# Kernel tuning notes

Hardware: AMD Instinct MI355X
Metric: run time of the kernel (lower is better)

Reference implementation:

```python
import jax, jax.numpy as jnp
import numpy as np

B, I, O, G = 262144, 3, 64, 128


def setup_inputs() -> dict:
    key = jax.random.key(0)
    kx, kc = jax.random.split(key)
    x = jax.random.uniform(kx, (1, B, I), dtype=jnp.float32)  # coords in [0,1)
    coeffs = jax.random.normal(kc, (2, O, I, G), dtype=jnp.float32) / (
        np.float32(np.sqrt(I) * np.sqrt(G))
    )
    bias = jnp.zeros((1, O), dtype=jnp.float32)
    return {"x": x, "coeffs": coeffs, "bias": bias}


def reference(x, coeffs, bias):
    # x: (1, B, I); coeffs: (2, O, I, G); bias: (1, O)
    b, i = x.shape[1], x.shape[2]
    two, o, _, g = coeffs.shape
    k = jnp.arange(1, g + 1, dtype=x.dtype)          # (G,)
    kx = x.reshape(b, i, 1) * k                      # (B, I, G)
    cosf = jnp.cos(kx).reshape(b, i * g)             # (B, I*G)
    sinf = jnp.sin(kx).reshape(b, i * g)             # (B, I*G)
    w = coeffs.reshape(2, o, i * g)                  # (2, O, I*G)
    # sum over (input_dim, gridsize) fused as one GEMM per trig branch
    out = cosf @ w[0].T + sinf @ w[1].T + bias       # (B, O)
    return out
```

## Files before the change

### kernel.cpp

```cpp
#include <hip/hip_runtime.h>
#include <hip/hip_bf16.h>

typedef __attribute__((ext_vector_type(8))) short short8;
typedef __attribute__((ext_vector_type(4))) float f32x4;
typedef __attribute__((ext_vector_type(2))) float f32x2;
typedef __attribute__((ext_vector_type(4))) unsigned int u32x4;

#define NROWS   262144
#define ODIM    64
#define NBLOCKS 256
#define TPB     1024
#define INV2PI  0.15915494309189535f

__device__ __forceinline__ float cos2pi(float f){ float r; asm("v_cos_f32 %0, %1" : "=v"(r) : "v"(f)); return r; }
__device__ __forceinline__ float sin2pi(float f){ float r; asm("v_sin_f32 %0, %1" : "=v"(r) : "v"(f)); return r; }
__device__ __forceinline__ unsigned pkbf(float lo, float hi){
    unsigned r; asm("v_cvt_pk_bf16_f32 %0, %1, %2" : "=v"(r) : "v"(lo), "v"(hi)); return r;
}
__device__ __forceinline__ short8 as_s8(u32x4 v){ union{u32x4 u; short8 s;} x; x.u = v; return x.s; }
__device__ __forceinline__ short bf16_of(float f){
    union { __hip_bfloat16 h; short s; } u; u.h = __float2bfloat16(f); return u.s;
}

extern "C" __global__ void __launch_bounds__(TPB, 4)
fourier_mfma(const float* __restrict__ x,
             const float* __restrict__ coeffs,
             const float* __restrict__ bias,
             float* __restrict__ out)
{
    __shared__ short8 Wlds[24 * 4 * 64];

    const int tid = threadIdx.x;

    for (int fl = tid; fl < 24*4*64; fl += TPB) {
        const int ks = fl >> 8;
        const int nt = (fl >> 6) & 3;
        const int ln = fl & 63;
        const int o  = nt*16 + (ln & 15);
        const int kg = ln >> 4;
        union { short8 v; short s[8]; } fr;
        #pragma unroll
        for (int h = 0; h < 2; ++h) {
            const int kb  = ks*32 + h*16;
            const int br  = (kb >= 384) ? 1 : 0;
            const int rem = kb - br*384;
            const int ii  = rem >> 7;
            const int g0  = (rem & 127) + kg*4;
            const float* wp = coeffs + (((br*ODIM + o)*3 + ii) << 7) + g0;
            #pragma unroll
            for (int j = 0; j < 4; ++j) fr.s[h*4 + j] = bf16_of(wp[j]);
        }
        Wlds[fl] = fr.v;
    }

    const int lane = tid & 63;
    const int wid  = tid >> 6;
    const int mrow = lane & 15;
    const int kgrp = lane >> 4;
    const float h0f = (float)(4*kgrp + 1);

    const int unit = blockIdx.x * 16 + wid;
    const int base = unit * 64;

    f32x2 xr[2][3];
    #pragma unroll
    for (int rg = 0; rg < 2; ++rg) {
        const int rowA = base + (rg*2 + 0)*16 + mrow;
        const int rowB = base + (rg*2 + 1)*16 + mrow;
        #pragma unroll
        for (int i = 0; i < 3; ++i)
            xr[rg][i] = (f32x2){ x[rowA*3 + i] * INV2PI, x[rowB*3 + i] * INV2PI };
    }
    float bcol[4];
    #pragma unroll
    for (int nt = 0; nt < 4; ++nt) bcol[nt] = bias[nt*16 + mrow];

    __syncthreads();

#define ANCHOR(RG, I) do {                                          \
    const f32x2 a = xr[RG][I];                                      \
    cv  = (f32x2){ cos2pi(a.x), cos2pi(a.y) };                      \
    sv  = (f32x2){ sin2pi(a.x), sin2pi(a.y) };                      \
    f32x2 t = (f32x2){ 16.f*a.x, 16.f*a.y };                        \
    t.x -= floorf(t.x); t.y -= floorf(t.y);                         \
    c16 = (f32x2){ cos2pi(t.x), cos2pi(t.y) };                      \
    s16 = (f32x2){ sin2pi(t.x), sin2pi(t.y) };                      \
    f32x2 u = (f32x2){ h0f*a.x, h0f*a.y };                          \
    u.x -= floorf(u.x); u.y -= floorf(u.y);                         \
    stc = (f32x2){ cos2pi(u.x), cos2pi(u.y) };                      \
    sts = (f32x2){ sin2pi(u.x), sin2pi(u.y) };                      \
} while (0)

#define HALF(D0, D1, FCA, FCB, FSA, FSB) do {                       \
    const f32x2 c0 = stc,        s0 = sts;                          \
    const f32x2 c1 = c0*cv - s0*sv, s1 = s0*cv + c0*sv;             \
    FCA.D0 = pkbf(c0.x, c1.x);  FCB.D0 = pkbf(c0.y, c1.y);          \
    FSA.D0 = pkbf(s0.x, s1.x);  FSB.D0 = pkbf(s0.y, s1.y);          \
    const f32x2 c2 = c1*cv - s1*sv, s2 = s1*cv + c1*sv;             \
    const f32x2 c3 = c2*cv - s2*sv, s3 = s2*cv + c2*sv;             \
    FCA.D1 = pkbf(c2.x, c3.x);  FCB.D1 = pkbf(c2.y, c3.y);          \
    FSA.D1 = pkbf(s2.x, s3.x);  FSB.D1 = pkbf(s2.y, s3.y);          \
    const f32x2 nc = stc*c16 - sts*s16, ns = sts*c16 + stc*s16;     \
    stc = nc; sts = ns;                                             \
} while (0)

#define FEAT(RG, KKP, FCA, FCB, FSA, FSB) do {                      \
    if (((KKP) & 3) == 0) ANCHOR(RG, (KKP) >> 2);                   \
    HALF(x, y, FCA, FCB, FSA, FSB);                                 \
    HALF(z, w, FCA, FCB, FSA, FSB);                                 \
} while (0)

    #pragma unroll
    for (int rg = 0; rg < 2; ++rg) {
        f32x4 acc[2][4];
        #pragma unroll
        for (int rr = 0; rr < 2; ++rr)
            #pragma unroll
            for (int nt = 0; nt < 4; ++nt)
                acc[rr][nt] = (f32x4){0.f, 0.f, 0.f, 0.f};

        f32x2 cv, sv, c16, s16, stc, sts;
        u32x4 F[2][4];

        FEAT(rg, 0, F[0][0], F[0][1], F[0][2], F[0][3]);

        #pragma unroll
        for (int kk = 0; kk < 12; ++kk) {
            const int cb = kk & 1;
            short8 bc[4], bs[4];
            #pragma unroll
            for (int nt = 0; nt < 4; ++nt) {
                bc[nt] = Wlds[(kk*4 + nt)*64 + lane];
                bs[nt] = Wlds[((kk + 12)*4 + nt)*64 + lane];
            }

            if (kk < 11)
                FEAT(rg, kk+1, F[cb^1][0], F[cb^1][1], F[cb^1][2], F[cb^1][3]);

            const short8 fAc = as_s8(F[cb][0]);
            const short8 fBc = as_s8(F[cb][1]);
            const short8 fAs = as_s8(F[cb][2]);
            const short8 fBs = as_s8(F[cb][3]);

            __builtin_amdgcn_s_setprio(1);
            #pragma unroll
            for (int nt = 0; nt < 4; ++nt) {
                acc[0][nt] = __builtin_amdgcn_mfma_f32_16x16x32_bf16(fAc, bc[nt], acc[0][nt], 0, 0, 0);
                acc[1][nt] = __builtin_amdgcn_mfma_f32_16x16x32_bf16(fBc, bc[nt], acc[1][nt], 0, 0, 0);
                acc[0][nt] = __builtin_amdgcn_mfma_f32_16x16x32_bf16(fAs, bs[nt], acc[0][nt], 0, 0, 0);
                acc[1][nt] = __builtin_amdgcn_mfma_f32_16x16x32_bf16(fBs, bs[nt], acc[1][nt], 0, 0, 0);
            }
            __builtin_amdgcn_s_setprio(0);
        }

        #pragma unroll
        for (int rr = 0; rr < 2; ++rr) {
            const int row0 = base + (rg*2 + rr)*16 + kgrp*4;
            #pragma unroll
            for (int nt = 0; nt < 4; ++nt) {
                #pragma unroll
                for (int q = 0; q < 4; ++q) {
                    out[(row0 + q)*ODIM + nt*16 + mrow] = acc[rr][nt][q] + bcol[nt];
                }
            }
        }
    }
#undef FEAT
#undef HALF
#undef ANCHOR
}

extern "C" void kernel_launch(void* const* d_in, const int* in_sizes, int n_in,
                              void* d_out, int out_size, void* d_ws, size_t ws_size,
                              hipStream_t stream) {
    const float* x      = (const float*)d_in[0];
    const float* coeffs = (const float*)d_in[1];
    const float* bias   = (const float*)d_in[2];
    float* out = (float*)d_out;
    (void)in_sizes; (void)n_in; (void)out_size; (void)d_ws; (void)ws_size;
    hipLaunchKernelGGL(fourier_mfma, dim3(NBLOCKS), dim3(TPB), 0, stream, x, coeffs, bias, out);
}
```

Baseline: 41.89 us.

## Use packed FMA for trig recurrence, drop feature double-buffer, regroup MFMAs

The angle-addition recurrence now uses explicit v_pk_mul_f32/v_pk_fma_f32 inline asm, so each step works on two rows with fewer VALU instructions. The double-buffered feature registers, which computed the next k-step's features during the current MFMAs, are removed. Features are now computed just before they are used. The MFMA issue order is regrouped so that consecutive MFMAs hit independent accumulators within each A operand group. This lowers register pressure and instruction count, but it loses the explicit software overlap between feature generation and the MFMAs.

```diff
diff --git a/kernel.cpp b/kernel.cpp
--- a/kernel.cpp
+++ b/kernel.cpp
@@ -14,13 +14,18 @@
 
 __device__ __forceinline__ float cos2pi(float f){ float r; asm("v_cos_f32 %0, %1" : "=v"(r) : "v"(f)); return r; }
 __device__ __forceinline__ float sin2pi(float f){ float r; asm("v_sin_f32 %0, %1" : "=v"(r) : "v"(f)); return r; }
+__device__ __forceinline__ f32x2 pk_mul(f32x2 a, f32x2 b){
+    f32x2 d; asm("v_pk_mul_f32 %0, %1, %2" : "=v"(d) : "v"(a), "v"(b)); return d; }
+__device__ __forceinline__ f32x2 pk_fma(f32x2 a, f32x2 b, f32x2 c){
+    f32x2 d; asm("v_pk_fma_f32 %0, %1, %2, %3" : "=v"(d) : "v"(a), "v"(b), "v"(c)); return d; }
+__device__ __forceinline__ f32x2 pk_fms(f32x2 a, f32x2 b, f32x2 c){
+    f32x2 d; asm("v_pk_fma_f32 %0, %1, %2, %3 neg_lo:[0,0,1] neg_hi:[0,0,1]"
+                 : "=v"(d) : "v"(a), "v"(b), "v"(c)); return d; }
 __device__ __forceinline__ unsigned pkbf(float lo, float hi){
-    unsigned r; asm("v_cvt_pk_bf16_f32 %0, %1, %2" : "=v"(r) : "v"(lo), "v"(hi)); return r;
-}
+    unsigned r; asm("v_cvt_pk_bf16_f32 %0, %1, %2" : "=v"(r) : "v"(lo), "v"(hi)); return r; }
 __device__ __forceinline__ short8 as_s8(u32x4 v){ union{u32x4 u; short8 s;} x; x.u = v; return x.s; }
 __device__ __forceinline__ short bf16_of(float f){
-    union { __hip_bfloat16 h; short s; } u; u.h = __float2bfloat16(f); return u.s;
-}
+    union { __hip_bfloat16 h; short s; } u; u.h = __float2bfloat16(f); return u.s; }
 
 extern "C" __global__ void __launch_bounds__(TPB, 4)
 fourier_mfma(const float* __restrict__ x,
@@ -91,23 +96,21 @@
     sts = (f32x2){ sin2pi(u.x), sin2pi(u.y) };                      \
 } while (0)
 
-#define HALF(D0, D1, FCA, FCB, FSA, FSB) do {                       \
-    const f32x2 c0 = stc,        s0 = sts;                          \
-    const f32x2 c1 = c0*cv - s0*sv, s1 = s0*cv + c0*sv;             \
+#define HALF(D0, D1) do {                                           \
+    const f32x2 c0 = stc, s0 = sts;                                 \
+    const f32x2 c1 = pk_fms(c0, cv, pk_mul(s0, sv));                \
+    const f32x2 s1 = pk_fma(s0, cv, pk_mul(c0, sv));                \
     FCA.D0 = pkbf(c0.x, c1.x);  FCB.D0 = pkbf(c0.y, c1.y);          \
     FSA.D0 = pkbf(s0.x, s1.x);  FSB.D0 = pkbf(s0.y, s1.y);          \
-    const f32x2 c2 = c1*cv - s1*sv, s2 = s1*cv + c1*sv;             \
-    const f32x2 c3 = c2*cv - s2*sv, s3 = s2*cv + c2*sv;             \
+    const f32x2 c2 = pk_fms(c1, cv, pk_mul(s1, sv));                \
+    const f32x2 s2 = pk_fma(s1, cv, pk_mul(c1, sv));                \
+    const f32x2 c3 = pk_fms(c2, cv, pk_mul(s2, sv));                \
+    const f32x2 s3 = pk_fma(s2, cv, pk_mul(c2, sv));                \
     FCA.D1 = pkbf(c2.x, c3.x);  FCB.D1 = pkbf(c2.y, c3.y);          \
     FSA.D1 = pkbf(s2.x, s3.x);  FSB.D1 = pkbf(s2.y, s3.y);          \
-    const f32x2 nc = stc*c16 - sts*s16, ns = sts*c16 + stc*s16;     \
+    const f32x2 nc = pk_fms(stc, c16, pk_mul(sts, s16));            \
+    const f32x2 ns = pk_fma(stc, s16, pk_mul(sts, c16));            \
     stc = nc; sts = ns;                                             \
-} while (0)
-
-#define FEAT(RG, KKP, FCA, FCB, FSA, FSB) do {                      \
-    if (((KKP) & 3) == 0) ANCHOR(RG, (KKP) >> 2);                   \
-    HALF(x, y, FCA, FCB, FSA, FSB);                                 \
-    HALF(z, w, FCA, FCB, FSA, FSB);                                 \
 } while (0)
 
     #pragma unroll
@@ -120,13 +123,9 @@
                 acc[rr][nt] = (f32x4){0.f, 0.f, 0.f, 0.f};
 
         f32x2 cv, sv, c16, s16, stc, sts;
-        u32x4 F[2][4];
-
-        FEAT(rg, 0, F[0][0], F[0][1], F[0][2], F[0][3]);
 
         #pragma unroll
         for (int kk = 0; kk < 12; ++kk) {
-            const int cb = kk & 1;
             short8 bc[4], bs[4];
             #pragma unroll
             for (int nt = 0; nt < 4; ++nt) {
@@ -134,22 +133,30 @@
                 bs[nt] = Wlds[((kk + 12)*4 + nt)*64 + lane];
             }
 
-            if (kk < 11)
-                FEAT(rg, kk+1, F[cb^1][0], F[cb^1][1], F[cb^1][2], F[cb^1][3]);
+            if ((kk & 3) == 0) ANCHOR(rg, kk >> 2);
 
-            const short8 fAc = as_s8(F[cb][0]);
-            const short8 fBc = as_s8(F[cb][1]);
-            const short8 fAs = as_s8(F[cb][2]);
-            const short8 fBs = as_s8(F[cb][3]);
+            u32x4 FCA, FCB, FSA, FSB;
+            HALF(x, y);
+            HALF(z, w);
+
+            const short8 fAc = as_s8(FCA);
+            const short8 fBc = as_s8(FCB);
+            const short8 fAs = as_s8(FSA);
+            const short8 fBs = as_s8(FSB);
 
             __builtin_amdgcn_s_setprio(1);
             #pragma unroll
-            for (int nt = 0; nt < 4; ++nt) {
+            for (int nt = 0; nt < 4; ++nt)
                 acc[0][nt] = __builtin_amdgcn_mfma_f32_16x16x32_bf16(fAc, bc[nt], acc[0][nt], 0, 0, 0);
+            #pragma unroll
+            for (int nt = 0; nt < 4; ++nt)
                 acc[1][nt] = __builtin_amdgcn_mfma_f32_16x16x32_bf16(fBc, bc[nt], acc[1][nt], 0, 0, 0);
+            #pragma unroll
+            for (int nt = 0; nt < 4; ++nt)
                 acc[0][nt] = __builtin_amdgcn_mfma_f32_16x16x32_bf16(fAs, bs[nt], acc[0][nt], 0, 0, 0);
+            #pragma unroll
+            for (int nt = 0; nt < 4; ++nt)
                 acc[1][nt] = __builtin_amdgcn_mfma_f32_16x16x32_bf16(fBs, bs[nt], acc[1][nt], 0, 0, 0);
-            }
             __builtin_amdgcn_s_setprio(0);
         }
 
@@ -165,7 +172,6 @@
             }
         }
     }
-#undef FEAT
 #undef HALF
 #undef ANCHOR
 }
```

Measured after the change: 41.68 us. No clear change (-0.5%).
